# Kernel optimization log

Measured on AMD Instinct MI355X. Metric: run time of the kernel, lower is better.

## Reference

```python
import jax, jax.numpy as jnp
import numpy as np
import math

D_MODEL = 1024
D_STATE = 16
D_CONV = 4
EXPAND = 2
D_INNER = EXPAND * D_MODEL  # 2048
DT_RANK = 64
B_SZ = 2
L_SEQ = 1024


def setup_inputs() -> dict:
    key = jax.random.key(0)
    ks = jax.random.split(key, 10)
    x = jax.random.normal(ks[0], (B_SZ, L_SEQ, D_MODEL), dtype=jnp.float32)
    in_proj_w = jax.random.normal(ks[1], (2 * D_INNER, D_MODEL), dtype=jnp.float32) * (1.0 / math.sqrt(D_MODEL))
    conv_w = jax.random.normal(ks[2], (D_INNER, 1, D_CONV), dtype=jnp.float32) * (1.0 / math.sqrt(D_CONV))
    conv_b = jax.random.normal(ks[3], (D_INNER,), dtype=jnp.float32) * 0.01
    x_proj_w = jax.random.normal(ks[4], (DT_RANK + 2 * D_STATE, D_INNER), dtype=jnp.float32) * (1.0 / math.sqrt(D_INNER))
    dt_init_std = DT_RANK ** (-0.5)
    dt_proj_w = jax.random.uniform(ks[5], (D_INNER, DT_RANK), dtype=jnp.float32, minval=-dt_init_std, maxval=dt_init_std)
    dt = jnp.exp(jax.random.uniform(ks[6], (D_INNER,), dtype=jnp.float32) * (math.log(0.1) - math.log(0.001)) + math.log(0.001))
    dt = jnp.clip(dt, 1e-4, None)
    dt_proj_b = dt + jnp.log(-jnp.expm1(-dt))
    A_log = jnp.log(jnp.tile(jnp.arange(1, D_STATE + 1, dtype=jnp.float32)[None, :], (D_INNER, 1)))
    D = jnp.ones((D_INNER,), dtype=jnp.float32)
    out_proj_w = jax.random.normal(ks[7], (D_MODEL, D_INNER), dtype=jnp.float32) * (1.0 / math.sqrt(D_INNER))
    return {"x": x, "in_proj_w": in_proj_w, "conv_w": conv_w, "conv_b": conv_b,
            "x_proj_w": x_proj_w, "dt_proj_w": dt_proj_w, "dt_proj_b": dt_proj_b,
            "A_log": A_log, "D": D, "out_proj_w": out_proj_w}


def _mamba_forward(x, in_proj_w, conv_w, conv_b, x_proj_w, dt_proj_w, dt_proj_b, A_log, D, out_proj_w):
    B, L, _ = x.shape
    # input projection -> x, z each [B, L, Di]
    xz = jnp.einsum('bld,ed->ble', x, in_proj_w)
    xs, z = jnp.split(xz, 2, axis=-1)
    # causal depthwise conv along L (torch pads K-1 both sides then trims -> left pad only)
    xc = jnp.transpose(xs, (0, 2, 1))  # [B, Di, L]
    xc = jax.lax.conv_general_dilated(
        xc, conv_w, window_strides=(1,), padding=[(D_CONV - 1, 0)],
        feature_group_count=D_INNER, dimension_numbers=('NCH', 'OIH', 'NCH'))
    xc = xc + conv_b[None, :, None]
    xs = jnp.transpose(xc, (0, 2, 1))  # [B, L, Di]
    xs = jax.nn.silu(xs)
    # SSM parameters
    A = -jnp.exp(A_log)  # [Di, N]
    dbc = jnp.einsum('bld,ed->ble', xs, x_proj_w)
    delta_r = dbc[..., :DT_RANK]
    Bm = dbc[..., DT_RANK:DT_RANK + D_STATE]       # [B, L, N]
    Cm = dbc[..., DT_RANK + D_STATE:]              # [B, L, N]
    delta = jnp.einsum('blr,dr->bld', delta_r, dt_proj_w)
    delta = jax.nn.softplus(delta + dt_proj_b)     # [B, L, Di]
    # selective scan: h_t = exp(delta*A)*h_{t-1} + delta*B*x
    dA = jnp.exp(delta[..., None] * A)                          # [B, L, Di, N]
    dBx = (delta * xs)[..., None] * Bm[:, :, None, :]           # [B, L, Di, N]
    dA_t = jnp.moveaxis(dA, 1, 0)    # [L, B, Di, N]
    dBx_t = jnp.moveaxis(dBx, 1, 0)
    C_t = jnp.moveaxis(Cm, 1, 0)     # [L, B, N]
    h0 = jnp.zeros((B, D_INNER, D_STATE), dtype=xs.dtype)

    def step(h, inp):
        da, bx, c = inp
        h = da * h + bx
        y = jnp.einsum('bdn,bn->bd', h, c)
        return h, y

    _, ys = jax.lax.scan(step, h0, (dA_t, dBx_t, C_t))
    y = jnp.moveaxis(ys, 0, 1)       # [B, L, Di]
    y = y + D * xs
    # gating and output projection
    out = y * jax.nn.silu(z)
    return jnp.einsum('bld,od->blo', out, out_proj_w)


def reference(x, in_proj_w, conv_w, conv_b, x_proj_w, dt_proj_w, dt_proj_b, A_log, D, out_proj_w):
    return _mamba_forward(x, in_proj_w, conv_w, conv_b, x_proj_w, dt_proj_w, dt_proj_b, A_log, D, out_proj_w)
```

## Files before the change

### kernel.cpp

```cpp
#include <hip/hip_runtime.h>
#include <hip/hip_bf16.h>

typedef __attribute__((ext_vector_type(8))) short short8;
typedef __attribute__((ext_vector_type(4))) float f32x4;
typedef __hip_bfloat16 bf16;

#define D_MODEL 1024
#define D_INNER 2048
#define DT_RANK 64
#define D_STATE 16
#define B_SZ 2
#define L_SEQ 1024
#define NSEG 32
#define SL 32

__device__ __forceinline__ float b2f(bf16 x){ return __bfloat162float(x); }
__device__ __forceinline__ bf16  f2b(float x){ return __float2bfloat16(x); }

__device__ __forceinline__ void cvt_store8(bf16* dst, const float* s){
  union { short8 v; bf16 e[8]; } u;
  #pragma unroll
  for (int i = 0; i < 8; i++) u.e[i] = f2b(s[i]);
  *(short8*)dst = u.v;
}

__device__ __forceinline__ void gl_lds16(const bf16* g, bf16* l){
  __builtin_amdgcn_global_load_lds((const __attribute__((address_space(1))) unsigned int*)g,
                                   (__attribute__((address_space(3))) unsigned int*)l, 16, 0, 0);
}

__global__ __launch_bounds__(256) void cvt5_k(const float* s0, bf16* d0, int c0,
                                              const float* s1, bf16* d1, int c1,
                                              const float* s2, bf16* d2, int c2,
                                              const float* s3, bf16* d3, int c3,
                                              const float* s4, bf16* d4, int c4)
{
  int i = blockIdx.x * 256 + threadIdx.x;
  const float* s; bf16* d; int off;
  if      (i < c0) { s = s0; d = d0; off = i; }
  else if (i < c1) { s = s1; d = d1; off = i - c0; }
  else if (i < c2) { s = s2; d = d2; off = i - c1; }
  else if (i < c3) { s = s3; d = d3; off = i - c2; }
  else if (i < c4) { s = s4; d = d4; off = i - c3; }
  else return;
  float b[8];
  *(float4*)&b[0] = *(const float4*)(s + (size_t)off * 8);
  *(float4*)&b[4] = *(const float4*)(s + (size_t)off * 8 + 4);
  cvt_store8(d + (size_t)off * 8, b);
}

template<int MODE, int JT>
__global__ __launch_bounds__(256) void gemm_glds(const bf16* __restrict__ A,
                                                 const bf16* __restrict__ B,
                                                 void* __restrict__ Cout,
                                                 int M, int N, int K)
{
  constexpr int BN = JT * 32;
  constexpr int BI = BN / 64;
  __shared__ bf16 As[128 * 32];
  __shared__ bf16 Bs[BN * 32];

  const int gx = gridDim.x;
  const int nwg = gx * gridDim.y;
  const int flat = blockIdx.y * gx + blockIdx.x;
  const int swz = (flat & 7) * (nwg >> 3) + (flat >> 3);
  const int bm = (swz / gx) * 128, bn = (swz % gx) * BN;

  const int tid  = threadIdx.x;
  const int lane = tid & 63, wave = tid >> 6;
  const int wm = (wave & 1) * 64, wn = (wave >> 1) * (JT * 16);
  const int r = lane & 15, q = lane >> 4;

  const bf16* asrc[2];
  #pragma unroll
  for (int i = 0; i < 2; i++) {
    int c = i * 256 + tid;
    asrc[i] = A + (size_t)(bm + (c >> 2)) * K + (c & 3) * 8;
  }
  const bf16* bsrc[BI];
  #pragma unroll
  for (int i = 0; i < BI; i++) {
    int c = i * 256 + tid;
    bsrc[i] = B + (size_t)(bn + (c >> 2)) * K + (c & 3) * 8;
  }

  f32x4 acc[4][JT];
  #pragma unroll
  for (int i = 0; i < 4; i++)
    #pragma unroll
    for (int j = 0; j < JT; j++) acc[i][j] = (f32x4){0.f,0.f,0.f,0.f};

  for (int k0 = 0; k0 < K; k0 += 32) {
    #pragma unroll
    for (int i = 0; i < 2; i++)
      gl_lds16(asrc[i] + k0, &As[(i * 256 + tid) * 8]);
    #pragma unroll
    for (int i = 0; i < BI; i++)
      gl_lds16(bsrc[i] + k0, &Bs[(i * 256 + tid) * 8]);
    __syncthreads();
    short8 af[4], bfr[JT];
    #pragma unroll
    for (int i = 0; i < 4; i++)  af[i]  = *(const short8*)&As[(wm + i*16 + r) * 32 + q*8];
    #pragma unroll
    for (int j = 0; j < JT; j++) bfr[j] = *(const short8*)&Bs[(wn + j*16 + r) * 32 + q*8];
    #pragma unroll
    for (int j = 0; j < JT; j++)
      #pragma unroll
      for (int i = 0; i < 4; i++)
        acc[i][j] = __builtin_amdgcn_mfma_f32_16x16x32_bf16(af[i], bfr[j], acc[i][j], 0, 0, 0);
    __syncthreads();
  }

  #pragma unroll
  for (int i = 0; i < 4; i++)
    #pragma unroll
    for (int j = 0; j < JT; j++)
      #pragma unroll
      for (int t = 0; t < 4; t++) {
        int row = bm + wm + i*16 + q*4 + t;
        int col = bn + wn + j*16 + r;
        float v = acc[i][j][t];
        if (MODE == 0) ((float*)Cout)[(size_t)row * N + col] = v;
        else           ((bf16*)Cout)[(size_t)row * N + col] = f2b(v);
      }
}

__global__ __launch_bounds__(256) void gemm_dt(const bf16* __restrict__ A,
                                               const bf16* __restrict__ W,
                                               float* __restrict__ Cout,
                                               const float* __restrict__ bias,
                                               int M, int N)
{
  __shared__ __align__(16) float stg[4][16][68];
  const int lane = threadIdx.x & 63, wave = threadIdx.x >> 6;
  const int ntg  = N >> 6;
  const int task = blockIdx.x * 4 + wave;
  const int mt   = task / ntg;
  const int ng   = task - mt * ntg;
  const int r = lane & 15, q = lane >> 4;

  const bf16* pa = A + (size_t)(mt*16 + r) * DT_RANK + q*8;
  short8 a0 = *(const short8*)pa;
  short8 a1 = *(const short8*)(pa + 32);

  #pragma unroll
  for (int j = 0; j < 4; j++) {
    const bf16* pb = W + (size_t)(ng*64 + j*16 + r) * DT_RANK + q*8;
    short8 b0 = *(const short8*)pb;
    short8 b1 = *(const short8*)(pb + 32);
    f32x4 c = {0.f,0.f,0.f,0.f};
    c = __builtin_amdgcn_mfma_f32_16x16x32_bf16(a0, b0, c, 0, 0, 0);
    c = __builtin_amdgcn_mfma_f32_16x16x32_bf16(a1, b1, c, 0, 0, 0);
    float bv = bias[ng*64 + j*16 + r];
    #pragma unroll
    for (int t = 0; t < 4; t++) {
      float xv = c[t] + bv;
      float sp = (xv > 20.f) ? xv : log1pf(__expf(xv));
      stg[wave][q*4 + t][j*16 + r] = sp;
    }
  }
  {
    int row = lane >> 2, q4 = lane & 3;
    const float* src = &stg[wave][row][q4 * 16];
    float4 w0 = *(const float4*)(src);
    float4 w1 = *(const float4*)(src + 4);
    float4 w2 = *(const float4*)(src + 8);
    float4 w3 = *(const float4*)(src + 12);
    float* gdst = Cout + (size_t)(mt*16 + row) * N + ng*64 + q4*16;
    *(float4*)(gdst)      = w0;
    *(float4*)(gdst + 4)  = w1;
    *(float4*)(gdst + 8)  = w2;
    *(float4*)(gdst + 12) = w3;
  }
}

__global__ __launch_bounds__(256) void gemm_xproj(const bf16* __restrict__ A,
                                                  const bf16* __restrict__ W,
                                                  float* __restrict__ dbc,
                                                  bf16* __restrict__ dr)
{
  const int K = D_INNER;
  const int lane = threadIdx.x & 63, wave = threadIdx.x >> 6;
  const int mt = blockIdx.y * 4 + wave;
  const int nt = blockIdx.x;
  const int r = lane & 15, q = lane >> 4;
  const bf16* pa = A + (size_t)(mt*16 + r) * K + q*8;
  const bf16* pb = W + (size_t)(nt*16 + r) * K + q*8;
  f32x4 a0 = {0.f,0.f,0.f,0.f}, a1 = a0, a2 = a0, a3 = a0;
  for (int k0 = 0; k0 < K; k0 += 128) {
    short8 x0 = *(const short8*)(pa + k0);
    short8 w0 = *(const short8*)(pb + k0);
    short8 x1 = *(const short8*)(pa + k0 + 32);
    short8 w1 = *(const short8*)(pb + k0 + 32);
    short8 x2 = *(const short8*)(pa + k0 + 64);
    short8 w2 = *(const short8*)(pb + k0 + 64);
    short8 x3 = *(const short8*)(pa + k0 + 96);
    short8 w3 = *(const short8*)(pb + k0 + 96);
    a0 = __builtin_amdgcn_mfma_f32_16x16x32_bf16(x0, w0, a0, 0, 0, 0);
    a1 = __builtin_amdgcn_mfma_f32_16x16x32_bf16(x1, w1, a1, 0, 0, 0);
    a2 = __builtin_amdgcn_mfma_f32_16x16x32_bf16(x2, w2, a2, 0, 0, 0);
    a3 = __builtin_amdgcn_mfma_f32_16x16x32_bf16(x3, w3, a3, 0, 0, 0);
  }
  f32x4 acc = (a0 + a1) + (a2 + a3);
  #pragma unroll
  for (int t = 0; t < 4; t++) {
    int row = mt*16 + q*4 + t;
    int col = nt*16 + r;
    dbc[(size_t)row * 96 + col] = acc[t];
    if (col < DT_RANK) dr[(size_t)row * DT_RANK + col] = f2b(acc[t]);
  }
}

__global__ __launch_bounds__(256) void conv_silu_k(const bf16* __restrict__ xz,
                                                   const float* __restrict__ cw,
                                                   const float* __restrict__ cb,
                                                   bf16* __restrict__ xs_b)
{
  int idx = blockIdx.x * 256 + threadIdx.x;
  int dg = idx & (D_INNER/8 - 1);
  int bl = idx >> 8;
  int l  = bl & (L_SEQ - 1);
  int d0 = dg * 8;
  const float4* cw4 = (const float4*)cw;
  float4 w[8];
  #pragma unroll
  for (int i = 0; i < 8; i++) w[i] = cw4[d0 + i];
  float acc[8];
  #pragma unroll
  for (int i = 0; i < 8; i++) acc[i] = cb[d0 + i];
  #pragma unroll
  for (int j = 0; j < 4; ++j) {
    int lp = l - 3 + j;
    if (lp >= 0) {
      short8 v = *(const short8*)(xz + (size_t)(bl - 3 + j) * (2*D_INNER) + d0);
      #pragma unroll
      for (int i = 0; i < 8; i++)
        acc[i] += ((const float*)&w[i])[j] * b2f(((const bf16*)&v)[i]);
    }
  }
  float o[8];
  #pragma unroll
  for (int i = 0; i < 8; i++) o[i] = acc[i] / (1.f + __expf(-acc[i]));
  cvt_store8(xs_b + (size_t)idx * 8, o);
}

__device__ __forceinline__ bool an_is_int(const float* An){
  bool f = true;
  #pragma unroll
  for (int n = 0; n < 16; n++) f = f & (fabsf(An[n] + (float)(n+1)) < 1e-3f);
  return f;
}

__global__ __launch_bounds__(256) void scan_pass1(const float* __restrict__ delta,
                                                  const bf16* __restrict__ xs,
                                                  const float* __restrict__ dbc,
                                                  const float* __restrict__ A_log,
                                                  float* __restrict__ hseg,
                                                  float* __restrict__ Stot)
{
  __shared__ float bcs[SL][32];
  const int d   = blockIdx.x * 256 + threadIdx.x;
  const int seg = blockIdx.y, b = blockIdx.z;
  for (int i = threadIdx.x; i < SL*32; i += 256) {
    int l = i >> 5, c = i & 31;
    bcs[l][c] = dbc[((size_t)b*L_SEQ + seg*SL + l)*96 + DT_RANK + c];
  }
  __syncthreads();
  float An[16], h[16];
  #pragma unroll
  for (int n = 0; n < 16; n++) { An[n] = -__expf(A_log[d*16 + n]); h[n] = 0.f; }
  float S = 0.f;
  if (an_is_int(An)) {
    for (int li = 0; li < SL; ++li) {
      size_t bl = (size_t)b * L_SEQ + seg*SL + li;
      float dv = delta[bl*D_INNER + d];
      float xv = b2f(xs[bl*D_INNER + d]);
      S += dv;
      float dx = dv * xv;
      float q = __expf(-dv), w = 1.f;
      #pragma unroll
      for (int n = 0; n < 16; n++) {
        w *= q;
        h[n] = w * h[n] + dx * bcs[li][n];
      }
    }
  } else {
    for (int li = 0; li < SL; ++li) {
      size_t bl = (size_t)b * L_SEQ + seg*SL + li;
      float dv = delta[bl*D_INNER + d];
      float xv = b2f(xs[bl*D_INNER + d]);
      S += dv;
      float dx = dv * xv;
      #pragma unroll
      for (int n = 0; n < 16; n++)
        h[n] = __expf(dv * An[n]) * h[n] + dx * bcs[li][n];
    }
  }
  float* hp = hseg + (((size_t)seg*B_SZ + b)*D_INNER + d) * 16;
  #pragma unroll
  for (int n = 0; n < 16; n++) hp[n] = h[n];
  Stot[((size_t)seg*B_SZ + b)*D_INNER + d] = S;
}

__global__ __launch_bounds__(256) void scan_combine(const float* __restrict__ Stot,
                                                    float* __restrict__ hseg,
                                                    const float* __restrict__ A_log)
{
  int idx = blockIdx.x * 256 + threadIdx.x;
  int n = idx & 15;
  int d = (idx >> 4) & (D_INNER - 1);
  int b = idx >> 15;
  float An = -__expf(A_log[d*16 + n]);
  float H = 0.f;
  for (int s = 0; s < NSEG; s++) {
    size_t base = ((size_t)s*B_SZ + b)*D_INNER + d;
    float St   = Stot[base];
    float hloc = hseg[base*16 + n];
    hseg[base*16 + n] = H;
    H = __expf(An*St)*H + hloc;
  }
}

__global__ __launch_bounds__(256) void scan_pass3(const float* __restrict__ delta,
                                                  const bf16* __restrict__ xs,
                                                  const float* __restrict__ dbc,
                                                  const float* __restrict__ A_log,
                                                  const float* __restrict__ hseg,
                                                  const bf16* __restrict__ xz,
                                                  const float* __restrict__ Dw,
                                                  bf16* __restrict__ outin)
{
  __shared__ float bcs[SL][32];
  const int d   = blockIdx.x * 256 + threadIdx.x;
  const int seg = blockIdx.y, b = blockIdx.z;
  for (int i = threadIdx.x; i < SL*32; i += 256) {
    int l = i >> 5, c = i & 31;
    bcs[l][c] = dbc[((size_t)b*L_SEQ + seg*SL + l)*96 + DT_RANK + c];
  }
  __syncthreads();
  float An[16], h[16];
  const float* hp = hseg + (((size_t)seg*B_SZ + b)*D_INNER + d) * 16;
  #pragma unroll
  for (int n = 0; n < 16; n++) { An[n] = -__expf(A_log[d*16 + n]); h[n] = hp[n]; }
  const float Dv = Dw[d];
  if (an_is_int(An)) {
    for (int li = 0; li < SL; ++li) {
      size_t bl = (size_t)b * L_SEQ + seg*SL + li;
      float dv = delta[bl*D_INNER + d];
      float xv = b2f(xs[bl*D_INNER + d]);
      float dx = dv * xv;
      float q = __expf(-dv), w = 1.f;
      float y = 0.f;
      #pragma unroll
      for (int n = 0; n < 16; n++) {
        w *= q;
        h[n] = w * h[n] + dx * bcs[li][n];
        y   += h[n] * bcs[li][16 + n];
      }
      y += Dv * xv;
      float z = b2f(xz[bl*(size_t)(2*D_INNER) + D_INNER + d]);
      float g = z / (1.f + __expf(-z));
      outin[bl*D_INNER + d] = f2b(y * g);
    }
  } else {
    for (int li = 0; li < SL; ++li) {
      size_t bl = (size_t)b * L_SEQ + seg*SL + li;
      float dv = delta[bl*D_INNER + d];
      float xv = b2f(xs[bl*D_INNER + d]);
      float dx = dv * xv;
      float y = 0.f;
      #pragma unroll
      for (int n = 0; n < 16; n++) {
        h[n] = __expf(dv * An[n]) * h[n] + dx * bcs[li][n];
        y   += h[n] * bcs[li][16 + n];
      }
      y += Dv * xv;
      float z = b2f(xz[bl*(size_t)(2*D_INNER) + D_INNER + d]);
      float g = z / (1.f + __expf(-z));
      outin[bl*D_INNER + d] = f2b(y * g);
    }
  }
}

extern "C" void kernel_launch(void* const* d_in, const int* in_sizes, int n_in,
                              void* d_out, int out_size, void* d_ws, size_t ws_size,
                              hipStream_t stream)
{
  const float* x      = (const float*)d_in[0];
  const float* in_w   = (const float*)d_in[1];
  const float* conv_w = (const float*)d_in[2];
  const float* conv_b = (const float*)d_in[3];
  const float* xp_w   = (const float*)d_in[4];
  const float* dt_w   = (const float*)d_in[5];
  const float* dt_b   = (const float*)d_in[6];
  const float* A_log  = (const float*)d_in[7];
  const float* Dw     = (const float*)d_in[8];
  const float* out_w  = (const float*)d_in[9];
  float* out = (float*)d_out;

  char* p = (char*)d_ws;
  bf16*  xz    = (bf16*)p;  p += (size_t)B_SZ*L_SEQ*2*D_INNER*2;
  bf16*  xs_b  = (bf16*)p;  p += (size_t)B_SZ*L_SEQ*D_INNER*2;
  float* dbc   = (float*)p; p += (size_t)B_SZ*L_SEQ*96*4;
  bf16*  dr    = (bf16*)p;  p += (size_t)B_SZ*L_SEQ*DT_RANK*2;
  float* delta = (float*)p; p += (size_t)B_SZ*L_SEQ*D_INNER*4;
  float* Stot  = (float*)p; p += (size_t)NSEG*B_SZ*D_INNER*4;
  bf16*  outin = (bf16*)p;  p += (size_t)B_SZ*L_SEQ*D_INNER*2;
  bf16*  xp_wb = (bf16*)p;  p += (size_t)(DT_RANK+2*D_STATE)*D_INNER*2;
  bf16*  dt_wb = (bf16*)p;  p += (size_t)D_INNER*DT_RANK*2;
  bf16*  ow_b  = (bf16*)p;  p += (size_t)D_MODEL*D_INNER*2;
  char* u = p;
  bf16*  xb    = (bf16*)u;
  bf16*  in_wb = (bf16*)(u + (size_t)B_SZ*L_SEQ*D_MODEL*2);
  float* hseg  = (float*)u;
  p += (size_t)B_SZ*L_SEQ*(D_MODEL + 2*D_INNER)*2;

  const int M = B_SZ * L_SEQ;

  cvt5_k<<<4256, 256, 0, stream>>>(x, xb, 262144,
                                   in_w, in_wb, 786432,
                                   xp_w, xp_wb, 811008,
                                   dt_w, dt_wb, 827392,
                                   out_w, ow_b, 1089536);
  gemm_glds<2,2><<<dim3(2*D_INNER/64, M/128), 256, 0, stream>>>(xb, in_wb, xz, M, 2*D_INNER, D_MODEL);
  conv_silu_k<<<(M*D_INNER/8)/256, 256, 0, stream>>>(xz, conv_w, conv_b, xs_b);
  gemm_xproj<<<dim3(6, M/64), 256, 0, stream>>>(xs_b, xp_wb, dbc, dr);
  gemm_dt<<<(M/16)*(D_INNER/64)/4, 256, 0, stream>>>(dr, dt_wb, delta, dt_b, M, D_INNER);
  scan_pass1<<<dim3(D_INNER/256, NSEG, B_SZ), 256, 0, stream>>>(delta, xs_b, dbc, A_log, hseg, Stot);
  scan_combine<<<(B_SZ*D_INNER*16)/256, 256, 0, stream>>>(Stot, hseg, A_log);
  scan_pass3<<<dim3(D_INNER/256, NSEG, B_SZ), 256, 0, stream>>>(delta, xs_b, dbc, A_log, hseg, xz, Dw, outin);
  gemm_glds<0,2><<<dim3(D_MODEL/64, M/128), 256, 0, stream>>>(outin, ow_b, out, M, D_MODEL, D_INNER);
}
```

Baseline: 255.3 us.

## Double GEMM K-tile with XOR-swizzled LDS and fold scan combine into pass3

The LDS GEMM now stages 64-wide K tiles instead of 32, using an XOR swizzle on 16-byte slots so the fragment reads avoid bank conflicts. This halves the number of barrier-separated iterations, at the cost of twice the shared memory per block. Separately, the scan_combine kernel is removed: each pass3 block now rebuilds its incoming state by walking all earlier segment summaries from hseg and Stot. That drops one kernel launch and its serial pass, but adds redundant work that grows linearly with segment index.

New measurement: 247.4 us. -3.1%, faster.

```diff
diff --git a/kernel.cpp b/kernel.cpp
--- a/kernel.cpp
+++ b/kernel.cpp
@@ -56,9 +56,10 @@
                                                  int M, int N, int K)
 {
   constexpr int BN = JT * 32;
-  constexpr int BI = BN / 64;
-  __shared__ bf16 As[128 * 32];
-  __shared__ bf16 Bs[BN * 32];
+  constexpr int AI = 4;
+  constexpr int BI = BN / 32;
+  __shared__ bf16 As[128 * 64];
+  __shared__ bf16 Bs[BN * 64];
 
   const int gx = gridDim.x;
   const int nwg = gx * gridDim.y;
@@ -70,18 +71,21 @@
   const int lane = tid & 63, wave = tid >> 6;
   const int wm = (wave & 1) * 64, wn = (wave >> 1) * (JT * 16);
   const int r = lane & 15, q = lane >> 4;
-
-  const bf16* asrc[2];
-  #pragma unroll
-  for (int i = 0; i < 2; i++) {
+  const int rx = r & 7;
+
+  const bf16* asrc[AI];
+  #pragma unroll
+  for (int i = 0; i < AI; i++) {
     int c = i * 256 + tid;
-    asrc[i] = A + (size_t)(bm + (c >> 2)) * K + (c & 3) * 8;
+    int row = c >> 3, sl = (c & 7) ^ (row & 7);
+    asrc[i] = A + (size_t)(bm + row) * K + sl * 8;
   }
   const bf16* bsrc[BI];
   #pragma unroll
   for (int i = 0; i < BI; i++) {
     int c = i * 256 + tid;
-    bsrc[i] = B + (size_t)(bn + (c >> 2)) * K + (c & 3) * 8;
+    int row = c >> 3, sl = (c & 7) ^ (row & 7);
+    bsrc[i] = B + (size_t)(bn + row) * K + sl * 8;
   }
 
   f32x4 acc[4][JT];
@@ -90,24 +94,29 @@
     #pragma unroll
     for (int j = 0; j < JT; j++) acc[i][j] = (f32x4){0.f,0.f,0.f,0.f};
 
-  for (int k0 = 0; k0 < K; k0 += 32) {
-    #pragma unroll
-    for (int i = 0; i < 2; i++)
+  for (int k0 = 0; k0 < K; k0 += 64) {
+    #pragma unroll
+    for (int i = 0; i < AI; i++)
       gl_lds16(asrc[i] + k0, &As[(i * 256 + tid) * 8]);
     #pragma unroll
     for (int i = 0; i < BI; i++)
       gl_lds16(bsrc[i] + k0, &Bs[(i * 256 + tid) * 8]);
     __syncthreads();
-    short8 af[4], bfr[JT];
-    #pragma unroll
-    for (int i = 0; i < 4; i++)  af[i]  = *(const short8*)&As[(wm + i*16 + r) * 32 + q*8];
-    #pragma unroll
-    for (int j = 0; j < JT; j++) bfr[j] = *(const short8*)&Bs[(wn + j*16 + r) * 32 + q*8];
-    #pragma unroll
-    for (int j = 0; j < JT; j++)
+    #pragma unroll
+    for (int ks = 0; ks < 2; ks++) {
+      short8 af[4], bfr[JT];
       #pragma unroll
       for (int i = 0; i < 4; i++)
-        acc[i][j] = __builtin_amdgcn_mfma_f32_16x16x32_bf16(af[i], bfr[j], acc[i][j], 0, 0, 0);
+        af[i]  = *(const short8*)&As[(wm + i*16 + r) * 64 + ((q + ks*4) ^ rx) * 8];
+      #pragma unroll
+      for (int j = 0; j < JT; j++)
+        bfr[j] = *(const short8*)&Bs[(wn + j*16 + r) * 64 + ((q + ks*4) ^ rx) * 8];
+      #pragma unroll
+      for (int j = 0; j < JT; j++)
+        #pragma unroll
+        for (int i = 0; i < 4; i++)
+          acc[i][j] = __builtin_amdgcn_mfma_f32_16x16x32_bf16(af[i], bfr[j], acc[i][j], 0, 0, 0);
+    }
     __syncthreads();
   }
 
@@ -302,30 +311,12 @@
   Stot[((size_t)seg*B_SZ + b)*D_INNER + d] = S;
 }
 
-__global__ __launch_bounds__(256) void scan_combine(const float* __restrict__ Stot,
-                                                    float* __restrict__ hseg,
-                                                    const float* __restrict__ A_log)
-{
-  int idx = blockIdx.x * 256 + threadIdx.x;
-  int n = idx & 15;
-  int d = (idx >> 4) & (D_INNER - 1);
-  int b = idx >> 15;
-  float An = -__expf(A_log[d*16 + n]);
-  float H = 0.f;
-  for (int s = 0; s < NSEG; s++) {
-    size_t base = ((size_t)s*B_SZ + b)*D_INNER + d;
-    float St   = Stot[base];
-    float hloc = hseg[base*16 + n];
-    hseg[base*16 + n] = H;
-    H = __expf(An*St)*H + hloc;
-  }
-}
-
 __global__ __launch_bounds__(256) void scan_pass3(const float* __restrict__ delta,
                                                   const bf16* __restrict__ xs,
                                                   const float* __restrict__ dbc,
                                                   const float* __restrict__ A_log,
                                                   const float* __restrict__ hseg,
+                                                  const float* __restrict__ Stot,
                                                   const bf16* __restrict__ xz,
                                                   const float* __restrict__ Dw,
                                                   bf16* __restrict__ outin)
@@ -339,11 +330,41 @@
   }
   __syncthreads();
   float An[16], h[16];
-  const float* hp = hseg + (((size_t)seg*B_SZ + b)*D_INNER + d) * 16;
-  #pragma unroll
-  for (int n = 0; n < 16; n++) { An[n] = -__expf(A_log[d*16 + n]); h[n] = hp[n]; }
+  #pragma unroll
+  for (int n = 0; n < 16; n++) { An[n] = -__expf(A_log[d*16 + n]); h[n] = 0.f; }
+  const bool fast = an_is_int(An);
+
+  if (fast) {
+    for (int s = 0; s < seg; ++s) {
+      size_t base = ((size_t)s*B_SZ + b)*D_INNER + d;
+      float St = Stot[base];
+      const float4* hp4 = (const float4*)(hseg + base*16);
+      float4 e0 = hp4[0], e1 = hp4[1], e2 = hp4[2], e3 = hp4[3];
+      float he[16] = {e0.x,e0.y,e0.z,e0.w, e1.x,e1.y,e1.z,e1.w,
+                      e2.x,e2.y,e2.z,e2.w, e3.x,e3.y,e3.z,e3.w};
+      float qs = __expf(-St), w = 1.f;
+      #pragma unroll
+      for (int n = 0; n < 16; n++) {
+        w *= qs;
+        h[n] = w * h[n] + he[n];
+      }
+    }
+  } else {
+    for (int s = 0; s < seg; ++s) {
+      size_t base = ((size_t)s*B_SZ + b)*D_INNER + d;
+      float St = Stot[base];
+      const float4* hp4 = (const float4*)(hseg + base*16);
+      float4 e0 = hp4[0], e1 = hp4[1], e2 = hp4[2], e3 = hp4[3];
+      float he[16] = {e0.x,e0.y,e0.z,e0.w, e1.x,e1.y,e1.z,e1.w,
+                      e2.x,e2.y,e2.z,e2.w, e3.x,e3.y,e3.z,e3.w};
+      #pragma unroll
+      for (int n = 0; n < 16; n++)
+        h[n] = __expf(An[n]*St) * h[n] + he[n];
+    }
+  }
+
   const float Dv = Dw[d];
-  if (an_is_int(An)) {
+  if (fast) {
     for (int li = 0; li < SL; ++li) {
       size_t bl = (size_t)b * L_SEQ + seg*SL + li;
       float dv = delta[bl*D_INNER + d];
@@ -427,7 +448,6 @@
   gemm_xproj<<<dim3(6, M/64), 256, 0, stream>>>(xs_b, xp_wb, dbc, dr);
   gemm_dt<<<(M/16)*(D_INNER/64)/4, 256, 0, stream>>>(dr, dt_wb, delta, dt_b, M, D_INNER);
   scan_pass1<<<dim3(D_INNER/256, NSEG, B_SZ), 256, 0, stream>>>(delta, xs_b, dbc, A_log, hseg, Stot);
-  scan_combine<<<(B_SZ*D_INNER*16)/256, 256, 0, stream>>>(Stot, hseg, A_log);
-  scan_pass3<<<dim3(D_INNER/256, NSEG, B_SZ), 256, 0, stream>>>(delta, xs_b, dbc, A_log, hseg, xz, Dw, outin);
+  scan_pass3<<<dim3(D_INNER/256, NSEG, B_SZ), 256, 0, stream>>>(delta, xs_b, dbc, A_log, hseg, Stot, xz, Dw, outin);
   gemm_glds<0,2><<<dim3(D_MODEL/64, M/128), 256, 0, stream>>>(outin, ow_b, out, M, D_MODEL, D_INNER);
 }
```
